# Performance work log

Hardware: AMD Instinct MI355X
Metric: run time of the kernel (lower is better)

Reference implementation:

```python
import jax, jax.numpy as jnp
import numpy as np

N_NODES = 100000
N_EDGES = 3200000
D_FEAT = 128
N_LAYERS = 2

def setup_inputs() -> dict:
    key = jax.random.key(0)
    k1, k2, k3, k4 = jax.random.split(key, 4)
    x = jax.random.normal(k1, (N_NODES, D_FEAT), dtype=jnp.float32)
    edge_row = jax.random.randint(k2, (N_EDGES,), 0, N_NODES)  # destination (spmm output row)
    edge_col = jax.random.randint(k3, (N_EDGES,), 0, N_NODES)  # source node
    edge_vals = jax.random.uniform(k4, (N_EDGES,), dtype=jnp.float32)
    scalars = jnp.ones((N_LAYERS,), dtype=jnp.float32)  # per-layer learned scalar (init ones)
    return {"x": x, "edge_row": edge_row, "edge_col": edge_col,
            "edge_vals": edge_vals, "scalars": scalars}

def reference(x, edge_row, edge_col, edge_vals, scalars):
    # ScalarSGC forward with dropout p=0 (identity). Same adjacency each layer.
    for l in range(N_LAYERS):
        h = scalars[l] * x                      # scalar * x
        msg = edge_vals[:, None] * h[edge_col]  # [E, D] gather + scale
        agg = jax.ops.segment_sum(msg, edge_row, num_segments=N_NODES)  # spmm
        x = jax.nn.elu(agg)
    return x
```

## Files before the change

kernel.cpp:

```cpp
#include <hip/hip_runtime.h>
#include <math.h>
#include <stdint.h>


#define D_FEAT 128
#define D2     64
#define SCAN_TILE 1024

#define PB 256
#define PT 1024
#define RB_BITS 9
#define ROWS_PER_BUCKET 512
#define COL_BITS 17
#define CACHE_CAP 17152

__device__ __forceinline__ uint32_t f2bf(float f) {
    uint32_t u = __float_as_uint(f);
    return (u + 0x7FFFu + ((u >> 16) & 1u)) >> 16;
}
__device__ __forceinline__ float bf_lo(uint32_t w) { return __uint_as_float(w << 16); }
__device__ __forceinline__ float bf_hi(uint32_t w) { return __uint_as_float(w & 0xFFFF0000u); }

__global__ void convert_kernel(const float2* __restrict__ xin, uint32_t* __restrict__ xbf, int n2) {
    int i = blockIdx.x * blockDim.x + threadIdx.x;
    if (i < n2) {
        float2 f = xin[i];
        xbf[i] = f2bf(f.x) | (f2bf(f.y) << 16);
    }
}

__global__ __launch_bounds__(PT) void coarse_count_kernel(const int* __restrict__ row,
                                                          int* __restrict__ cnt,
                                                          int E, int nbuck) {
    __shared__ int hist[256];
    const int t = threadIdx.x;
    if (t < 256) hist[t] = 0;
    __syncthreads();
    const int stride = PB * PT;
    for (int i = blockIdx.x * PT + t; i < E; i += stride)
        atomicAdd(&hist[row[i] >> RB_BITS], 1);
    __syncthreads();
    if (t < nbuck) cnt[t * PB + blockIdx.x] = hist[t];
}

__global__ __launch_bounds__(SCAN_TILE) void scan1_kernel(const int* __restrict__ counts,
                                                          int* __restrict__ excl,
                                                          int* __restrict__ tileSums, int n) {
    __shared__ int wsum[16];
    const int tid  = threadIdx.x;
    const int lane = tid & 63;
    const int wave = tid >> 6;
    const int i    = blockIdx.x * SCAN_TILE + tid;

    int v = (i < n) ? counts[i] : 0;
    int incl = v;
    #pragma unroll
    for (int off = 1; off < 64; off <<= 1) {
        int t = __shfl_up(incl, off, 64);
        if (lane >= off) incl += t;
    }
    if (lane == 63) wsum[wave] = incl;
    __syncthreads();
    if (wave == 0) {
        int s = (lane < 16) ? wsum[lane] : 0;
        #pragma unroll
        for (int off = 1; off < 16; off <<= 1) {
            int t = __shfl_up(s, off, 64);
            if (lane >= off) s += t;
        }
        if (lane < 16) wsum[lane] = s;
    }
    __syncthreads();
    int wbase = (wave == 0) ? 0 : wsum[wave - 1];
    if (i < n) excl[i] = wbase + (incl - v);
    if (tid == 0) tileSums[blockIdx.x] = wsum[15];
}

__global__ __launch_bounds__(1024) void scan2_kernel(const int* __restrict__ tileSums,
                                                     int* __restrict__ tileBase,
                                                     int* __restrict__ total_out, int nb) {
    __shared__ int buf[1024];
    const int tid = threadIdx.x;
    int v = (tid < nb) ? tileSums[tid] : 0;
    buf[tid] = v;
    __syncthreads();
    #pragma unroll
    for (int off = 1; off < 1024; off <<= 1) {
        int t = (tid >= off) ? buf[tid - off] : 0;
        __syncthreads();
        buf[tid] += t;
        __syncthreads();
    }
    if (tid < nb) tileBase[tid] = buf[tid] - v;
    if (tid == nb - 1) *total_out = buf[tid];
}

__global__ __launch_bounds__(PT) void partition_kernel(const int* __restrict__ row,
                                                       const int* __restrict__ col,
                                                       const float* __restrict__ val,
                                                       const int* __restrict__ cnt,
                                                       const int* __restrict__ tileBase,
                                                       int2* __restrict__ pack2,
                                                       int E, int nbuck) {
    __shared__ int cur[256];
    const int t = threadIdx.x;
    if (t < nbuck) {
        int idx = t * PB + blockIdx.x;
        cur[t] = cnt[idx] + tileBase[idx >> 10];
    }
    __syncthreads();
    const int stride = PB * PT;
    for (int i = blockIdx.x * PT + t; i < E; i += stride) {
        int r = row[i];
        int pos = atomicAdd(&cur[r >> RB_BITS], 1);
        pack2[pos] = make_int2(col[i] | ((r & (ROWS_PER_BUCKET - 1)) << COL_BITS),
                               __float_as_int(val[i]));
    }
}

__global__ __launch_bounds__(1024) void fine_sort_kernel(const int* __restrict__ cnt,
                                                         const int* __restrict__ tileBase,
                                                         const int2* __restrict__ pack2,
                                                         int2* __restrict__ pack,
                                                         int* __restrict__ offsets,
                                                         int E, int N, int nbuck) {
    extern __shared__ int2 ecache[];
    __shared__ int buf[1024];
    __shared__ int cur[ROWS_PER_BUCKET];
    const int b = blockIdx.x;
    const int t = threadIdx.x;
    const int start = cnt[b << 8] + tileBase[b >> 2];
    const int end   = (b == nbuck - 1) ? E : (cnt[(b + 1) << 8] + tileBase[(b + 1) >> 2]);
    const int n  = end - start;
    const int nc = (n < CACHE_CAP) ? n : CACHE_CAP;

    for (int i = t; i < nc; i += 1024) ecache[i] = pack2[start + i];
    buf[t] = 0;
    __syncthreads();

    for (int i = t; i < n; i += 1024) {
        int key = (i < nc) ? ecache[i].x : pack2[start + i].x;
        atomicAdd(&buf[((unsigned)key) >> COL_BITS], 1);
    }
    __syncthreads();

    int v = buf[t];
    for (int off = 1; off < 1024; off <<= 1) {
        int tv = (t >= off) ? buf[t - off] : 0;
        __syncthreads();
        buf[t] += tv;
        __syncthreads();
    }
    int excl = buf[t] - v;
    if (t < ROWS_PER_BUCKET) {
        int r = (b << RB_BITS) + t;
        if (r < N) offsets[r] = start + excl;
        cur[t] = excl;
    }
    if (b == 0 && t == 0) offsets[N] = E;
    __syncthreads();

    for (int i = t; i < n; i += 1024) {
        int2 w = (i < nc) ? ecache[i] : pack2[start + i];
        int lr = ((unsigned)w.x) >> COL_BITS;
        int p = atomicAdd(&cur[lr], 1);
        pack[start + p] = make_int2(w.x & ((1 << COL_BITS) - 1), w.y);
    }
}

template <int OUT_BF16>
__global__ __launch_bounds__(256) void spmm_elu_kernel(
    const int* __restrict__ offsets, const int2* __restrict__ pack,
    const uint32_t* __restrict__ xin, void* __restrict__ xout,
    const float* __restrict__ scalars, int layer, int N) {
    const int wave = threadIdx.x >> 6;
    const uint32_t lane = threadIdx.x & 63;
    const int r    = blockIdx.x * 4 + wave;
    if (r >= N) return;

    int e = offsets[r];
    const int end = offsets[r + 1];

    float a0x = 0.f, a0y = 0.f, a1x = 0.f, a1y = 0.f;
    float a2x = 0.f, a2y = 0.f, a3x = 0.f, a3y = 0.f;

    for (; e + 4 <= end; e += 4) {
        int2 p0 = pack[e], p1 = pack[e + 1], p2 = pack[e + 2], p3 = pack[e + 3];
        uint32_t w0 = xin[(((uint32_t)p0.x) << 6) + lane];
        uint32_t w1 = xin[(((uint32_t)p1.x) << 6) + lane];
        uint32_t w2 = xin[(((uint32_t)p2.x) << 6) + lane];
        uint32_t w3 = xin[(((uint32_t)p3.x) << 6) + lane];
        float v0 = __int_as_float(p0.y), v1 = __int_as_float(p1.y);
        float v2 = __int_as_float(p2.y), v3 = __int_as_float(p3.y);
        a0x += v0 * bf_lo(w0); a0y += v0 * bf_hi(w0);
        a1x += v1 * bf_lo(w1); a1y += v1 * bf_hi(w1);
        a2x += v2 * bf_lo(w2); a2y += v2 * bf_hi(w2);
        a3x += v3 * bf_lo(w3); a3y += v3 * bf_hi(w3);
    }
    for (; e < end; ++e) {
        int2 p = pack[e];
        uint32_t w = xin[(((uint32_t)p.x) << 6) + lane];
        float v = __int_as_float(p.y);
        a0x += v * bf_lo(w); a0y += v * bf_hi(w);
    }

    float ax = (a0x + a1x) + (a2x + a3x);
    float ay = (a0y + a1y) + (a2y + a3y);
    const float s = scalars[layer];
    ax *= s; ay *= s;
    ax = (ax > 0.f) ? ax : (expf(ax) - 1.f);
    ay = (ay > 0.f) ? ay : (expf(ay) - 1.f);

    if (OUT_BF16) {
        ((uint32_t*)xout)[(size_t)r * D2 + lane] = f2bf(ax) | (f2bf(ay) << 16);
    } else {
        ((float2*)xout)[(size_t)r * D2 + lane] = make_float2(ax, ay);
    }
}

extern "C" void kernel_launch(void* const* d_in, const int* in_sizes, int n_in,
                              void* d_out, int out_size, void* d_ws, size_t ws_size,
                              hipStream_t stream) {
    const float* x         = (const float*)d_in[0];
    const int*   edge_row  = (const int*)d_in[1];
    const int*   edge_col  = (const int*)d_in[2];
    const float* edge_vals = (const float*)d_in[3];
    const float* scalars   = (const float*)d_in[4];

    const int N = in_sizes[0] / D_FEAT;
    const int E = in_sizes[1];
    const int nbuck = (N + ROWS_PER_BUCKET - 1) >> RB_BITS;
    const int M = nbuck * PB;
    const int NB = (M + SCAN_TILE - 1) / SCAN_TILE;

    char*  ws  = (char*)d_ws;
    size_t off = 0;
    auto alloc = [&](size_t bytes) -> void* {
        off = (off + 255) & ~(size_t)255;
        void* p = ws + off;
        off += bytes;
        return p;
    };
    int*      offsets  = (int*)alloc((size_t)(N + 1) * sizeof(int));
    int*      cnt      = (int*)alloc((size_t)(M + 1) * sizeof(int));
    int*      tileSums = (int*)alloc((size_t)NB * sizeof(int));
    int*      tileBase = (int*)alloc((size_t)NB * sizeof(int));
    int2*     pack2    = (int2*)alloc((size_t)E * sizeof(int2));
    int2*     pack     = (int2*)alloc((size_t)E * sizeof(int2));
    uint32_t* xbf      = (uint32_t*)alloc((size_t)N * D2 * sizeof(uint32_t));
    uint32_t* hbf      = (uint32_t*)pack2;
    (void)ws_size;

    convert_kernel<<<(N * D2 + 255) / 256, 256, 0, stream>>>((const float2*)x, xbf, N * D2);
    coarse_count_kernel<<<PB, PT, 0, stream>>>(edge_row, cnt, E, nbuck);
    scan1_kernel<<<NB, SCAN_TILE, 0, stream>>>(cnt, cnt, tileSums, M);
    scan2_kernel<<<1, 1024, 0, stream>>>(tileSums, tileBase, cnt + M, NB);
    partition_kernel<<<PB, PT, 0, stream>>>(edge_row, edge_col, edge_vals, cnt, tileBase,
                                            pack2, E, nbuck);
    fine_sort_kernel<<<nbuck, 1024, (size_t)CACHE_CAP * sizeof(int2), stream>>>(
        cnt, tileBase, pack2, pack, offsets, E, N, nbuck);

    const int nblk = (N + 3) / 4;
    spmm_elu_kernel<1><<<nblk, 256, 0, stream>>>(offsets, pack, xbf, hbf, scalars, 0, N);
    spmm_elu_kernel<0><<<nblk, 256, 0, stream>>>(offsets, pack, hbf, (void*)d_out, scalars, 1, N);
}
```

Baseline: 436.6 us.

## Slice edges by source column range to improve gather cache locality in SpMM

The fine sort now bins each row's edges into eight slices by source-column range, producing per-(row,slice) offsets. Each SpMM wave processes a fixed group of up to 25 rows slice by slice, so that gathers across many rows hit a narrower band of the feature matrix at a time and reuse cache better. The conversion and coarse count kernels are fused into one launch, and buckets shrink to 256 rows to fit the larger bin array in shared memory. The cost is 25-row register accumulators per wave, more offset reads, and a fixed wave count that assumes N/4096 stays at or below 25.

Measured after the change: 875.6 us. +100.5%, slower.

```diff
diff --git a/kernel.cpp b/kernel.cpp
--- a/kernel.cpp
+++ b/kernel.cpp
@@ -9,10 +9,18 @@
 
 #define PB 256
 #define PT 1024
-#define RB_BITS 9
-#define ROWS_PER_BUCKET 512
+#define RB_BITS 8
+#define ROWS_PER_BUCKET 256
 #define COL_BITS 17
-#define CACHE_CAP 17152
+#define SLICE_BITS 3
+#define NSLICE 8
+#define SLICE_SHIFT 14
+#define FINE_BINS (ROWS_PER_BUCKET << SLICE_BITS)
+#define CACHE_CAP 9216
+
+#define SPMM_BLOCKS 1024
+#define SPMM_WAVES  4096
+#define MAX_ROWS_PER_WAVE 25
 
 __device__ __forceinline__ uint32_t f2bf(float f) {
     uint32_t u = __float_as_uint(f);
@@ -21,22 +29,19 @@
 __device__ __forceinline__ float bf_lo(uint32_t w) { return __uint_as_float(w << 16); }
 __device__ __forceinline__ float bf_hi(uint32_t w) { return __uint_as_float(w & 0xFFFF0000u); }
 
-__global__ void convert_kernel(const float2* __restrict__ xin, uint32_t* __restrict__ xbf, int n2) {
-    int i = blockIdx.x * blockDim.x + threadIdx.x;
-    if (i < n2) {
+__global__ __launch_bounds__(PT) void convert_count_kernel(
+    const float2* __restrict__ xin, uint32_t* __restrict__ xbf, int n2,
+    const int* __restrict__ row, int* __restrict__ cnt, int E, int nbuck) {
+    __shared__ int hist[512];
+    const int t = threadIdx.x;
+    if (t < 512) hist[t] = 0;
+
+    const int stride = PB * PT;
+    for (int i = blockIdx.x * PT + t; i < n2; i += stride) {
         float2 f = xin[i];
         xbf[i] = f2bf(f.x) | (f2bf(f.y) << 16);
     }
-}
-
-__global__ __launch_bounds__(PT) void coarse_count_kernel(const int* __restrict__ row,
-                                                          int* __restrict__ cnt,
-                                                          int E, int nbuck) {
-    __shared__ int hist[256];
-    const int t = threadIdx.x;
-    if (t < 256) hist[t] = 0;
-    __syncthreads();
-    const int stride = PB * PT;
+    __syncthreads();
     for (int i = blockIdx.x * PT + t; i < E; i += stride)
         atomicAdd(&hist[row[i] >> RB_BITS], 1);
     __syncthreads();
@@ -102,7 +107,7 @@
                                                        const int* __restrict__ tileBase,
                                                        int2* __restrict__ pack2,
                                                        int E, int nbuck) {
-    __shared__ int cur[256];
+    __shared__ int cur[512];
     const int t = threadIdx.x;
     if (t < nbuck) {
         int idx = t * PB + blockIdx.x;
@@ -122,11 +127,11 @@
                                                          const int* __restrict__ tileBase,
                                                          const int2* __restrict__ pack2,
                                                          int2* __restrict__ pack,
-                                                         int* __restrict__ offsets,
-                                                         int E, int N, int nbuck) {
-    extern __shared__ int2 ecache[];
-    __shared__ int buf[1024];
-    __shared__ int cur[ROWS_PER_BUCKET];
+                                                         int* __restrict__ offsets2,
+                                                         int E, int nbuck) {
+    __shared__ int2 ecache[CACHE_CAP];
+    __shared__ int  bins[FINE_BINS];
+    __shared__ int  sbuf[1024];
     const int b = blockIdx.x;
     const int t = threadIdx.x;
     const int start = cnt[b << 8] + tileBase[b >> 2];
@@ -135,86 +140,101 @@
     const int nc = (n < CACHE_CAP) ? n : CACHE_CAP;
 
     for (int i = t; i < nc; i += 1024) ecache[i] = pack2[start + i];
-    buf[t] = 0;
+    bins[t] = 0; bins[t + 1024] = 0;
     __syncthreads();
 
     for (int i = t; i < n; i += 1024) {
         int key = (i < nc) ? ecache[i].x : pack2[start + i].x;
-        atomicAdd(&buf[((unsigned)key) >> COL_BITS], 1);
-    }
-    __syncthreads();
-
-    int v = buf[t];
+        int bin = ((key >> COL_BITS) << SLICE_BITS) | ((key >> SLICE_SHIFT) & (NSLICE - 1));
+        atomicAdd(&bins[bin], 1);
+    }
+    __syncthreads();
+
+    int c0 = bins[2 * t], c1 = bins[2 * t + 1];
+    int pair = c0 + c1;
+    sbuf[t] = pair;
+    __syncthreads();
     for (int off = 1; off < 1024; off <<= 1) {
-        int tv = (t >= off) ? buf[t - off] : 0;
-        __syncthreads();
-        buf[t] += tv;
-        __syncthreads();
-    }
-    int excl = buf[t] - v;
-    if (t < ROWS_PER_BUCKET) {
-        int r = (b << RB_BITS) + t;
-        if (r < N) offsets[r] = start + excl;
-        cur[t] = excl;
-    }
-    if (b == 0 && t == 0) offsets[N] = E;
+        int tv = (t >= off) ? sbuf[t - off] : 0;
+        __syncthreads();
+        sbuf[t] += tv;
+        __syncthreads();
+    }
+    int pexcl = sbuf[t] - pair;
+    int a0 = start + pexcl, a1 = start + pexcl + c0;
+    bins[2 * t]     = a0;
+    bins[2 * t + 1] = a1;
+    const int gbase = b << (RB_BITS + SLICE_BITS);
+    offsets2[gbase + 2 * t]     = a0;
+    offsets2[gbase + 2 * t + 1] = a1;
+    if (b == 0 && t == 0) offsets2[nbuck << (RB_BITS + SLICE_BITS)] = E;
     __syncthreads();
 
     for (int i = t; i < n; i += 1024) {
         int2 w = (i < nc) ? ecache[i] : pack2[start + i];
-        int lr = ((unsigned)w.x) >> COL_BITS;
-        int p = atomicAdd(&cur[lr], 1);
-        pack[start + p] = make_int2(w.x & ((1 << COL_BITS) - 1), w.y);
+        int bin = ((w.x >> COL_BITS) << SLICE_BITS) | ((w.x >> SLICE_SHIFT) & (NSLICE - 1));
+        int p = atomicAdd(&bins[bin], 1);
+        pack[p] = make_int2(w.x & ((1 << COL_BITS) - 1), w.y);
     }
 }
 
 template <int OUT_BF16>
-__global__ __launch_bounds__(256) void spmm_elu_kernel(
-    const int* __restrict__ offsets, const int2* __restrict__ pack,
+__global__ __launch_bounds__(256, 4) void spmm_elu_kernel(
+    const int* __restrict__ offs2, const int2* __restrict__ pack,
     const uint32_t* __restrict__ xin, void* __restrict__ xout,
     const float* __restrict__ scalars, int layer, int N) {
-    const int wave = threadIdx.x >> 6;
+    const int wid  = blockIdx.x * 4 + (threadIdx.x >> 6);
     const uint32_t lane = threadIdx.x & 63;
-    const int r    = blockIdx.x * 4 + wave;
-    if (r >= N) return;
-
-    int e = offsets[r];
-    const int end = offsets[r + 1];
-
-    float a0x = 0.f, a0y = 0.f, a1x = 0.f, a1y = 0.f;
-    float a2x = 0.f, a2y = 0.f, a3x = 0.f, a3y = 0.f;
-
-    for (; e + 4 <= end; e += 4) {
-        int2 p0 = pack[e], p1 = pack[e + 1], p2 = pack[e + 2], p3 = pack[e + 3];
-        uint32_t w0 = xin[(((uint32_t)p0.x) << 6) + lane];
-        uint32_t w1 = xin[(((uint32_t)p1.x) << 6) + lane];
-        uint32_t w2 = xin[(((uint32_t)p2.x) << 6) + lane];
-        uint32_t w3 = xin[(((uint32_t)p3.x) << 6) + lane];
-        float v0 = __int_as_float(p0.y), v1 = __int_as_float(p1.y);
-        float v2 = __int_as_float(p2.y), v3 = __int_as_float(p3.y);
-        a0x += v0 * bf_lo(w0); a0y += v0 * bf_hi(w0);
-        a1x += v1 * bf_lo(w1); a1y += v1 * bf_hi(w1);
-        a2x += v2 * bf_lo(w2); a2y += v2 * bf_hi(w2);
-        a3x += v3 * bf_lo(w3); a3y += v3 * bf_hi(w3);
-    }
-    for (; e < end; ++e) {
-        int2 p = pack[e];
-        uint32_t w = xin[(((uint32_t)p.x) << 6) + lane];
-        float v = __int_as_float(p.y);
-        a0x += v * bf_lo(w); a0y += v * bf_hi(w);
-    }
-
-    float ax = (a0x + a1x) + (a2x + a3x);
-    float ay = (a0y + a1y) + (a2y + a3y);
-    const float s = scalars[layer];
-    ax *= s; ay *= s;
-    ax = (ax > 0.f) ? ax : (expf(ax) - 1.f);
-    ay = (ay > 0.f) ? ay : (expf(ay) - 1.f);
-
-    if (OUT_BF16) {
-        ((uint32_t*)xout)[(size_t)r * D2 + lane] = f2bf(ax) | (f2bf(ay) << 16);
-    } else {
-        ((float2*)xout)[(size_t)r * D2 + lane] = make_float2(ax, ay);
+    const int q   = N / SPMM_WAVES;
+    const int rem = N - q * SPMM_WAVES;
+    const int base = wid * q + (wid < rem ? wid : rem);
+    const int nr   = q + (wid < rem ? 1 : 0);
+
+    float ax[MAX_ROWS_PER_WAVE], ay[MAX_ROWS_PER_WAVE];
+    #pragma unroll
+    for (int k = 0; k < MAX_ROWS_PER_WAVE; ++k) { ax[k] = 0.f; ay[k] = 0.f; }
+
+    for (int s = 0; s < NSLICE; ++s) {
+        #pragma unroll
+        for (int k = 0; k < MAX_ROWS_PER_WAVE; ++k) {
+            if (k >= nr) break;
+            const int r = base + k;
+            int e        = offs2[(r << SLICE_BITS) + s];
+            const int e1 = offs2[(r << SLICE_BITS) + s + 1];
+            float sx = 0.f, sy = 0.f;
+            float tx = 0.f, ty = 0.f;
+            for (; e + 2 <= e1; e += 2) {
+                int2 p0 = pack[e], p1 = pack[e + 1];
+                uint32_t w0 = xin[(((uint32_t)p0.x) << 6) + lane];
+                uint32_t w1 = xin[(((uint32_t)p1.x) << 6) + lane];
+                float v0 = __int_as_float(p0.y), v1 = __int_as_float(p1.y);
+                sx += v0 * bf_lo(w0); sy += v0 * bf_hi(w0);
+                tx += v1 * bf_lo(w1); ty += v1 * bf_hi(w1);
+            }
+            if (e < e1) {
+                int2 p = pack[e];
+                uint32_t w = xin[(((uint32_t)p.x) << 6) + lane];
+                float v = __int_as_float(p.y);
+                sx += v * bf_lo(w); sy += v * bf_hi(w);
+            }
+            ax[k] += sx + tx;
+            ay[k] += sy + ty;
+        }
+    }
+
+    const float sc = scalars[layer];
+    #pragma unroll
+    for (int k = 0; k < MAX_ROWS_PER_WAVE; ++k) {
+        if (k >= nr) break;
+        const int r = base + k;
+        float vx = ax[k] * sc, vy = ay[k] * sc;
+        vx = (vx > 0.f) ? vx : (expf(vx) - 1.f);
+        vy = (vy > 0.f) ? vy : (expf(vy) - 1.f);
+        if (OUT_BF16) {
+            ((uint32_t*)xout)[((uint32_t)r << 6) + lane] = f2bf(vx) | (f2bf(vy) << 16);
+        } else {
+            ((float2*)xout)[((uint32_t)r << 6) + lane] = make_float2(vx, vy);
+        }
     }
 }
 
@@ -232,6 +252,7 @@
     const int nbuck = (N + ROWS_PER_BUCKET - 1) >> RB_BITS;
     const int M = nbuck * PB;
     const int NB = (M + SCAN_TILE - 1) / SCAN_TILE;
+    const int NOFF = (nbuck << (RB_BITS + SLICE_BITS)) + 1;
 
     char*  ws  = (char*)d_ws;
     size_t off = 0;
@@ -241,7 +262,7 @@
         off += bytes;
         return p;
     };
-    int*      offsets  = (int*)alloc((size_t)(N + 1) * sizeof(int));
+    int*      offsets2 = (int*)alloc((size_t)NOFF * sizeof(int));
     int*      cnt      = (int*)alloc((size_t)(M + 1) * sizeof(int));
     int*      tileSums = (int*)alloc((size_t)NB * sizeof(int));
     int*      tileBase = (int*)alloc((size_t)NB * sizeof(int));
@@ -251,16 +272,17 @@
     uint32_t* hbf      = (uint32_t*)pack2;
     (void)ws_size;
 
-    convert_kernel<<<(N * D2 + 255) / 256, 256, 0, stream>>>((const float2*)x, xbf, N * D2);
-    coarse_count_kernel<<<PB, PT, 0, stream>>>(edge_row, cnt, E, nbuck);
+    convert_count_kernel<<<PB, PT, 0, stream>>>((const float2*)x, xbf, N * D2,
+                                                edge_row, cnt, E, nbuck);
     scan1_kernel<<<NB, SCAN_TILE, 0, stream>>>(cnt, cnt, tileSums, M);
     scan2_kernel<<<1, 1024, 0, stream>>>(tileSums, tileBase, cnt + M, NB);
     partition_kernel<<<PB, PT, 0, stream>>>(edge_row, edge_col, edge_vals, cnt, tileBase,
                                             pack2, E, nbuck);
-    fine_sort_kernel<<<nbuck, 1024, (size_t)CACHE_CAP * sizeof(int2), stream>>>(
-        cnt, tileBase, pack2, pack, offsets, E, N, nbuck);
-
-    const int nblk = (N + 3) / 4;
-    spmm_elu_kernel<1><<<nblk, 256, 0, stream>>>(offsets, pack, xbf, hbf, scalars, 0, N);
-    spmm_elu_kernel<0><<<nblk, 256, 0, stream>>>(offsets, pack, hbf, (void*)d_out, scalars, 1, N);
-}
+    fine_sort_kernel<<<nbuck, 1024, 0, stream>>>(cnt, tileBase, pack2, pack, offsets2,
+                                                 E, nbuck);
+
+    spmm_elu_kernel<1><<<SPMM_BLOCKS, 256, 0, stream>>>(offsets2, pack, xbf, hbf,
+                                                        scalars, 0, N);
+    spmm_elu_kernel<0><<<SPMM_BLOCKS, 256, 0, stream>>>(offsets2, pack, hbf, (void*)d_out,
+                                                        scalars, 1, N);
+}
```
